# Optimization experiments

Measured on AMD Instinct MI355X. Metric: run time of the kernel, lower is better.

The kernel has to match this reference:

```python
import jax, jax.numpy as jnp
import numpy as np

N, E, IN_DIM, HID, HEADS, OUT_DIM, T = 50000, 200000, 32, 64, 4, 32, 3
NEG_SLOPE = 0.2  # PyG GATv2Conv default


def setup_inputs() -> dict:
    key = jax.random.key(0)
    ks = jax.random.split(key, 16)
    s = 0.1
    return {
        "feat": jax.random.normal(ks[0], (N, IN_DIM), jnp.float32),
        "W_in": jax.random.normal(ks[1], (IN_DIM, HID), jnp.float32) * s,
        "b_in": jnp.zeros((HID,), jnp.float32),
        "Wl": jax.random.normal(ks[2], (2 * HID, HEADS * HID), jnp.float32) * s,
        "bl": jnp.zeros((HEADS * HID,), jnp.float32),
        "Wr": jax.random.normal(ks[3], (2 * HID, HEADS * HID), jnp.float32) * s,
        "br": jnp.zeros((HEADS * HID,), jnp.float32),
        "att": jax.random.normal(ks[4], (HEADS, HID), jnp.float32) * s,
        "b_conv": jnp.zeros((HEADS * HID,), jnp.float32),
        "Wg": jax.random.normal(ks[5], (HID, OUT_DIM), jnp.float32) * s,
        "bg": jnp.zeros((OUT_DIM,), jnp.float32),
        "edge_index": jax.random.randint(ks[6], (2, E), 0, N, jnp.int32),
        "node_mask": jax.random.randint(ks[7], (N,), 0, T + 1, jnp.int32),
        "current_state": jax.random.randint(ks[8], (N,), 0, 2, jnp.int32),
    }


def reference(feat, W_in, b_in, Wl, bl, Wr, br, att, b_conv, Wg, bg,
              edge_index, node_mask, current_state):
    # add self loops (GATv2Conv add_self_loops=True)
    loops = jnp.arange(N, dtype=edge_index.dtype)
    src = jnp.concatenate([edge_index[0], loops])  # [E+N]
    dst = jnp.concatenate([edge_index[1], loops])

    h0 = feat @ W_in + b_in  # [N, HID]
    bias_sum = b_conv.reshape(HEADS, HID).sum(0)  # heads are summed after bias add

    def step(h, i):
        active = node_mask > i  # [N] bool: nodes updated at this step
        x = jnp.concatenate([h, h0], axis=-1)  # [N, 2*HID]
        xl = (x @ Wl + bl).reshape(N, HEADS, HID)  # source transform
        xr = (x @ Wr + br).reshape(N, HEADS, HID)  # target transform
        e_act = active[src] & active[dst]  # edge alive iff both endpoints active
        s = jax.nn.leaky_relu(xl[src] + xr[dst], NEG_SLOPE)  # [E+N, H, C]
        score = jnp.einsum('ehc,hc->eh', s, att)  # [E+N, H]
        score = jnp.where(e_act[:, None], score, -1e30)
        smax = jax.lax.stop_gradient(
            jax.ops.segment_max(score, dst, num_segments=N))  # [N, H]
        ex = jnp.exp(score - smax[dst]) * e_act[:, None].astype(score.dtype)
        denom = jax.ops.segment_sum(ex, dst, num_segments=N)  # [N, H]
        alpha = ex / jnp.maximum(denom[dst], 1e-16)  # segment softmax per dst
        msg = alpha[:, :, None] * xl[src]  # [E+N, H, C]
        agg = jax.ops.segment_sum(msg, dst, num_segments=N)  # [N, H, C]
        out = jnp.tanh(agg.sum(1) + bias_sum)  # sum over heads, then Tanh
        return jnp.where(active[:, None], out, h), None

    h, _ = jax.lax.scan(step, h0, jnp.arange(T))
    # original returns g_embed(h[current_state]); fixed-shape variant: mask rows
    out = (h @ Wg + bg) * (current_state[:, None] > 0).astype(h.dtype)
    return out
```

## Files before the change

### kernel.cpp

```cpp
#include <hip/hip_runtime.h>
#include <hip/hip_bf16.h>

#define NN      50000
#define EE      200000
#define IN_DIM  32
#define HID     64
#define HEADS   4
#define OUTD    32
#define TSTEPS  3

typedef unsigned short bf16_t;
typedef __attribute__((ext_vector_type(8))) short  short8;
typedef __attribute__((ext_vector_type(4))) float  floatx4;

__device__ __forceinline__ float b2f(bf16_t u) {
    union { unsigned int i; float f; } v; v.i = ((unsigned int)u) << 16; return v.f;
}
__device__ __forceinline__ bf16_t f2b(float f) {
    union { float f; unsigned int i; } v; v.f = f;
    unsigned int r = v.i + 0x7FFF + ((v.i >> 16) & 1);
    return (bf16_t)(r >> 16);
}

#define DPP_ADD(x, ctrl) ((x) + __int_as_float(                                 \
        __builtin_amdgcn_update_dpp(0, __float_as_int(x), (ctrl), 0xF, 0xF, true)))

#define H0_BLOCKS ((NN + 63) / 64)
#define NB_NODE   ((NN + 255) / 256)
#define NBC       (NB_NODE * 4)
#define EB        ((EE + 1023) / 1024)

__global__ __launch_bounds__(256) void k_setup(
        const void* W_in, const void* b_in, const void* att, const void* bconv,
        const void* Wg, const void* bg,
        const void* Wl_raw, const void* Wr_raw, const void* bl_raw, const void* br_raw,
        const void* feat_raw, const int* __restrict__ nmask,
        const int* __restrict__ e_src, const int* __restrict__ e_dst,
        float* attf, float* bcf, float* Wgf, float* bgf,
        bf16_t* __restrict__ Wt, bf16_t* __restrict__ WtS, float* __restrict__ bb,
        int* __restrict__ deg4, int* __restrict__ flag, int* __restrict__ bcount,
        bf16_t* __restrict__ h0, bf16_t* __restrict__ h) {
    __shared__ int bad;
    __shared__ float Ws[IN_DIM * HID];
    __shared__ float bs[HID];
    __shared__ int wcnt[4][4];
    int t = threadIdx.x, bid = blockIdx.x;
    if (t == 0) bad = 0;
    __syncthreads();
    {
        const bf16_t* p = (const bf16_t*)W_in;
        int mybad = 0;
        for (int i = t; i < IN_DIM * HID; i += 256) {
            float v = b2f(p[i]);
            if (v != v || fabsf(v) > 100.f) mybad = 1;
        }
        if (mybad) atomicOr(&bad, 1);
    }
    __syncthreads();
    int f = bad ? 0 : 1;
    if (bid == 0 && t == 0) *flag = f;

    if (bid < 256) {
        int i = bid * 256 + t;
        int n = i >> 7, k = i & 127;
        const void* W = (n < 256) ? Wl_raw : Wr_raw;
        int nn = (n < 256) ? n : n - 256;
        float v = f ? b2f(((const bf16_t*)W)[k * 256 + nn])
                    : ((const float*)W)[k * 256 + nn];
        Wt[n * 128 + k] = f2b(v);
        if (k < 64) {
            float v2 = f ? b2f(((const bf16_t*)W)[(k + 64) * 256 + nn])
                         : ((const float*)W)[(k + 64) * 256 + nn];
            WtS[n * 64 + k] = f2b(v + v2);
        }
        if (k == 0) {
            const void* b = (n < 256) ? bl_raw : br_raw;
            bb[n] = f ? b2f(((const bf16_t*)b)[nn]) : ((const float*)b)[nn];
        }
    } else if (bid < 267) {
        int i = (bid - 256) * 256 + t;
        const void* src; float* dst; int off;
        if      (i < 256)  { src = att;   dst = attf; off = i; }
        else if (i < 512)  { src = bconv; dst = bcf;  off = i - 256; }
        else if (i < 2560) { src = Wg;    dst = Wgf;  off = i - 512; }
        else if (i < 2592) { src = bg;    dst = bgf;  off = i - 2560; }
        else return;
        dst[off] = f ? b2f(((const bf16_t*)src)[off]) : ((const float*)src)[off];
    } else if (bid < 267 + NB_NODE) {
        int nb = bid - 267;
        int i = nb * 256 + t;
        bool valid = i < NN;
        int wid = t >> 6, lane = t & 63;
        int v = 0;
        if (valid) { int m = nmask[i]; v = m < 0 ? 0 : (m > 3 ? 3 : m); }
#pragma unroll
        for (int b = 0; b < 4; b++) {
            unsigned long long mm = __ballot(valid && v == b);
            if (lane == 0) wcnt[wid][b] = __popcll(mm);
        }
        __syncthreads();
        if (t < 4)
            bcount[nb * 4 + t] = wcnt[0][t] + wcnt[1][t] + wcnt[2][t] + wcnt[3][t];
    } else if (bid < 267 + NB_NODE + EB) {
        int nb = bid - 267 - NB_NODE;
        int i = (nb * 256 + t) * 4;
        if (i + 3 < EE) {
            int4 dv = *(const int4*)(e_dst + i);
            int4 sv = *(const int4*)(e_src + i);
            int m0 = nmask[sv.x]; m0 = m0 < 0 ? 0 : (m0 > 3 ? 3 : m0);
            int m1 = nmask[sv.y]; m1 = m1 < 0 ? 0 : (m1 > 3 ? 3 : m1);
            int m2 = nmask[sv.z]; m2 = m2 < 0 ? 0 : (m2 > 3 ? 3 : m2);
            int m3 = nmask[sv.w]; m3 = m3 < 0 ? 0 : (m3 > 3 ? 3 : m3);
            atomicAdd(&deg4[dv.x * 4 + m0], 1);
            atomicAdd(&deg4[dv.y * 4 + m1], 1);
            atomicAdd(&deg4[dv.z * 4 + m2], 1);
            atomicAdd(&deg4[dv.w * 4 + m3], 1);
        } else {
            for (; i < EE; i++) {
                int s = e_src[i];
                int m = nmask[s]; m = m < 0 ? 0 : (m > 3 ? 3 : m);
                atomicAdd(&deg4[e_dst[i] * 4 + m], 1);
            }
        }
    } else {
        for (int i = t; i < IN_DIM * HID; i += 256)
            Ws[i] = f ? b2f(((const bf16_t*)W_in)[i]) : ((const float*)W_in)[i];
        if (t < HID)
            bs[t] = f ? b2f(((const bf16_t*)b_in)[t]) : ((const float*)b_in)[t];
        __syncthreads();
        int nb = bid - (267 + NB_NODE + EB);
        int wid = t >> 6, c = t & 63;
#pragma unroll
        for (int g = 0; g < 16; g++) {
            int node = (nb * 16 + g) * 4 + wid;
            if (node >= NN) break;
            float acc = bs[c];
            if (f) {
                const short8* fr8 = (const short8*)((const bf16_t*)feat_raw
                                                    + (size_t)node * IN_DIM);
#pragma unroll
                for (int j = 0; j < 4; j++) {
                    short8 fv = fr8[j];
#pragma unroll
                    for (int k = 0; k < 8; k++)
                        acc += b2f((bf16_t)fv[k]) * Ws[(j * 8 + k) * HID + c];
                }
            } else {
                const float4* fr4 = (const float4*)((const float*)feat_raw
                                                    + (size_t)node * IN_DIM);
#pragma unroll
                for (int j = 0; j < 8; j++) {
                    float4 fv = fr4[j];
                    acc += fv.x * Ws[(j * 4 + 0) * HID + c];
                    acc += fv.y * Ws[(j * 4 + 1) * HID + c];
                    acc += fv.z * Ws[(j * 4 + 2) * HID + c];
                    acc += fv.w * Ws[(j * 4 + 3) * HID + c];
                }
            }
            bf16_t o = f2b(acc);
            h0[(size_t)node * HID + c] = o;
            h [(size_t)node * HID + c] = o;
        }
    }
}

__global__ __launch_bounds__(256) void k_scan(const int* __restrict__ deg4,
                                              int* __restrict__ cur4,
                                              int* __restrict__ rend4,
                                              const int* __restrict__ bcount,
                                              int* __restrict__ mbuf,
                                              int n, int nch) {
    __shared__ int sc[256];
    __shared__ int spre[256];
    __shared__ int cb[4];
    int t = threadIdx.x, bid = blockIdx.x;

    if (bid == 0) {
        if (t < 4) cb[t] = 0;
        __syncthreads();
        for (int i = t; i < NBC; i += 256) atomicAdd(&cb[i & 3], bcount[i]);
        __syncthreads();
        if (t == 0) {
            int c1 = cb[1], c2 = cb[2], c3 = cb[3];
            mbuf[7] = 0;
            mbuf[6] = c3;
            mbuf[5] = c3 + c2;
            mbuf[4] = c3 + c2 + c1;
            mbuf[8] = c3 + c2 + c1;
            mbuf[9] = c3 + c2;
            mbuf[10] = c3;
        }
    }

    const int4* d4 = (const int4*)deg4;
    int base = bid * 1024;
    int pre = 0;
    for (int i = t; i < base; i += 256) {
        int4 q = d4[i];
        pre += q.x + q.y + q.z + q.w;
    }
    spre[t] = pre; __syncthreads();
    for (int off = 128; off > 0; off >>= 1) {
        if (t < off) spre[t] += spre[t + off];
        __syncthreads();
    }
    int bpref = spre[0];

    int4 dd[4]; int tot[4]; int s = 0;
#pragma unroll
    for (int j = 0; j < 4; j++) {
        int i = base + t * 4 + j;
        if (i < n) dd[j] = d4[i];
        else { dd[j].x = 0; dd[j].y = 0; dd[j].z = 0; dd[j].w = 0; }
        tot[j] = dd[j].x + dd[j].y + dd[j].z + dd[j].w;
        s += tot[j];
    }
    sc[t] = s; __syncthreads();
    for (int off = 1; off < 256; off <<= 1) {
        int add = (t >= off) ? sc[t - off] : 0;
        __syncthreads();
        sc[t] += add;
        __syncthreads();
    }
    int run = sc[t] - s + bpref;
#pragma unroll
    for (int j = 0; j < 4; j++) {
        int i = base + t * 4 + j;
        if (i < n) {
            int c3 = run;
            int c2 = c3 + dd[j].w;
            int c1 = c2 + dd[j].z;
            int c0 = c1 + dd[j].y;
            int4 cu; cu.x = c0; cu.y = c1; cu.z = c2; cu.w = c3;
            *(int4*)(cur4 + i * 4) = cu;
            int4 re; re.x = c0; re.y = c1; re.z = c2; re.w = run;
            *(int4*)(rend4 + i * 4) = re;
        }
        run += tot[j];
    }
}

__global__ __launch_bounds__(256) void k_scatter_all(const int* __restrict__ src,
                                                     const int* __restrict__ dst,
                                                     int* __restrict__ cur4,
                                                     int* __restrict__ col,
                                                     const int* __restrict__ mask,
                                                     int* __restrict__ mbuf,
                                                     int* __restrict__ order) {
    int t = threadIdx.x, bid = blockIdx.x;
    int i = bid * 256 + t;
    if (i < EE) {
        int sv = src[i];
        int m = mask[sv]; m = m < 0 ? 0 : (m > 3 ? 3 : m);
        int d = dst[i];
        int pos = atomicAdd(&cur4[d * 4 + m], 1);
        col[pos] = sv;
    }
    if (bid < NB_NODE) {
        __shared__ int wcnt[4][4];
        __shared__ int bbase[4];
        int wid = t >> 6, lane = t & 63;
        int ni = bid * 256 + t;
        bool valid = ni < NN;
        int v = 0;
        if (valid) { int m = mask[ni]; v = m < 0 ? 0 : (m > 3 ? 3 : m); }
        int rank = 0;
#pragma unroll
        for (int b = 0; b < 4; b++) {
            unsigned long long mm = __ballot(valid && v == b);
            if (valid && v == b)
                rank = __popcll(mm & ((lane == 0) ? 0ull : (~0ull >> (64 - lane))));
            if (lane == 0) wcnt[wid][b] = __popcll(mm);
        }
        __syncthreads();
        if (t < 4) {
            int tot = wcnt[0][t] + wcnt[1][t] + wcnt[2][t] + wcnt[3][t];
            bbase[t] = atomicAdd(&mbuf[4 + t], tot);
        }
        __syncthreads();
        if (valid) {
            int wpre = 0;
            for (int ww = 0; ww < wid; ww++) wpre += wcnt[ww][v];
            order[bbase[v] + wpre + rank] = ni;
        }
    }
}

__global__ __launch_bounds__(256) void k_gemm0(const bf16_t* __restrict__ h0,
                                               const bf16_t* __restrict__ WtS,
                                               const float* __restrict__ bb,
                                               bf16_t* __restrict__ xl,
                                               bf16_t* __restrict__ xr,
                                               const int* __restrict__ order,
                                               const int* __restrict__ mbuf) {
    int count = mbuf[8];
    int mbase = blockIdx.x * 64;
    if (mbase >= count) return;

    __shared__ bf16_t smem[64 * 72 + 128 * 72];
    bf16_t* As = smem;
    bf16_t* Bs = smem + 64 * 72;
    bf16_t* Cs = smem;

    int t = threadIdx.x;
    int nbase = blockIdx.y * 128;

    {
        int ln = t >> 2, lq = t & 3;
        int idx = mbase + ln;
        int node = (idx < count) ? order[idx] : -1;
        ulonglong2 z; z.x = 0; z.y = 0;
        ulonglong2 v0 = z, v1 = z;
        if (node >= 0) {
            v0 = *(const ulonglong2*)(h0 + (size_t)node * HID + lq * 16);
            v1 = *(const ulonglong2*)(h0 + (size_t)node * HID + lq * 16 + 8);
        }
        *(ulonglong2*)(&As[ln * 72 + lq * 16]) = v0;
        *(ulonglong2*)(&As[ln * 72 + lq * 16 + 8]) = v1;
    }
    {
        int n = t >> 1, kc = (t & 1) * 32;
        const bf16_t* srcp = WtS + (size_t)(nbase + n) * 64 + kc;
        bf16_t* dstp = &Bs[n * 72 + kc];
        *(ulonglong2*)(dstp)      = *(const ulonglong2*)(srcp);
        *(ulonglong2*)(dstp + 8)  = *(const ulonglong2*)(srcp + 8);
        *(ulonglong2*)(dstp + 16) = *(const ulonglong2*)(srcp + 16);
        *(ulonglong2*)(dstp + 24) = *(const ulonglong2*)(srcp + 24);
    }
    __syncthreads();

    int wv = t >> 6, lane = t & 63, mrow = lane & 15, quad = lane >> 4;
    floatx4 acc[8];
#pragma unroll
    for (int nf = 0; nf < 8; nf++) acc[nf] = (floatx4){0.f, 0.f, 0.f, 0.f};
#pragma unroll
    for (int kq = 0; kq < 2; kq++) {
        short8 a = *(const short8*)(&As[(wv * 16 + mrow) * 72 + kq * 32 + quad * 8]);
#pragma unroll
        for (int nf = 0; nf < 8; nf++) {
            short8 b = *(const short8*)(&Bs[(nf * 16 + mrow) * 72 + kq * 32 + quad * 8]);
            acc[nf] = __builtin_amdgcn_mfma_f32_16x16x32_bf16(a, b, acc[nf], 0, 0, 0);
        }
    }
    __syncthreads();

#pragma unroll
    for (int nf = 0; nf < 8; nf++) {
        float bv = bb[nbase + nf * 16 + mrow];
#pragma unroll
        for (int r = 0; r < 4; r++) {
            int m = wv * 16 + quad * 4 + r;
            Cs[m * 136 + nf * 16 + mrow] = f2b(acc[nf][r] + bv);
        }
    }
    __syncthreads();

    bf16_t* outp = (blockIdx.y < 2) ? xl : xr;
    int cc = (blockIdx.y & 1) * 128;
#pragma unroll
    for (int i = 0; i < 4; i++) {
        int c = t + i * 256;
        int m = c >> 4, kc = (c & 15) * 8;
        int idx = mbase + m;
        if (idx < count) {
            int node = order[idx];
            *(ulonglong2*)(outp + (size_t)node * 256 + cc + kc) =
                *(const ulonglong2*)(&Cs[m * 136 + kc]);
        }
    }
}

__global__ __launch_bounds__(256) void k_gemm_mfma(const bf16_t* __restrict__ h,
                                                   const bf16_t* __restrict__ h0,
                                                   const bf16_t* __restrict__ Wt,
                                                   const float* __restrict__ bb,
                                                   bf16_t* __restrict__ xl,
                                                   bf16_t* __restrict__ xr,
                                                   const int* __restrict__ order,
                                                   const int* __restrict__ mbuf,
                                                   int step) {
    int count = mbuf[8 + step];
    int mbase = blockIdx.x * 64;
    if (mbase >= count) return;

    __shared__ bf16_t smem[64 * 136 + 128 * 136];
    bf16_t* As = smem;
    bf16_t* Bs = smem + 64 * 136;
    bf16_t* Cs = smem;

    int t = threadIdx.x;
    int nbase = blockIdx.y * 128;

    {
        int ln = t >> 2, lq = t & 3;
        int idx = mbase + ln;
        int node = (idx < count) ? order[idx] : -1;
        ulonglong2 z; z.x = 0; z.y = 0;
#pragma unroll
        for (int j = 0; j < 2; j++) {
            int chunk = lq + j * 4;
            ulonglong2 vh = z, vh0 = z;
            if (node >= 0) {
                vh  = *(const ulonglong2*)(h  + (size_t)node * HID + chunk * 8);
                vh0 = *(const ulonglong2*)(h0 + (size_t)node * HID + chunk * 8);
            }
            *(ulonglong2*)(&As[ln * 136 + chunk * 8]) = vh;
            *(ulonglong2*)(&As[ln * 136 + 64 + chunk * 8]) = vh0;
        }
    }
#pragma unroll
    for (int i = 0; i < 8; i++) {
        int c = t + i * 256;
        int n = c >> 4, kc = (c & 15) * 8;
        *(ulonglong2*)(&Bs[n * 136 + kc]) =
            *(const ulonglong2*)(Wt + (size_t)(nbase + n) * 128 + kc);
    }
    __syncthreads();

    int wv = t >> 6, lane = t & 63, mrow = lane & 15, quad = lane >> 4;
    floatx4 acc[8];
#pragma unroll
    for (int nf = 0; nf < 8; nf++) acc[nf] = (floatx4){0.f, 0.f, 0.f, 0.f};
#pragma unroll
    for (int kq = 0; kq < 4; kq++) {
        short8 a = *(const short8*)(&As[(wv * 16 + mrow) * 136 + kq * 32 + quad * 8]);
#pragma unroll
        for (int nf = 0; nf < 8; nf++) {
            short8 b = *(const short8*)(&Bs[(nf * 16 + mrow) * 136 + kq * 32 + quad * 8]);
            acc[nf] = __builtin_amdgcn_mfma_f32_16x16x32_bf16(a, b, acc[nf], 0, 0, 0);
        }
    }
    __syncthreads();

#pragma unroll
    for (int nf = 0; nf < 8; nf++) {
        float bv = bb[nbase + nf * 16 + mrow];
#pragma unroll
        for (int r = 0; r < 4; r++) {
            int m = wv * 16 + quad * 4 + r;
            Cs[m * 136 + nf * 16 + mrow] = f2b(acc[nf][r] + bv);
        }
    }
    __syncthreads();

    bf16_t* outp = (blockIdx.y < 2) ? xl : xr;
    int cc = (blockIdx.y & 1) * 128;
#pragma unroll
    for (int i = 0; i < 4; i++) {
        int c = t + i * 256;
        int m = c >> 4, kc = (c & 15) * 8;
        int idx = mbase + m;
        if (idx < count) {
            int node = order[idx];
            *(ulonglong2*)(outp + (size_t)node * 256 + cc + kc) =
                *(const ulonglong2*)(&Cs[m * 136 + kc]);
        }
    }
}

__global__ __launch_bounds__(256) void k_agg(bf16_t* __restrict__ h,
                                             const bf16_t* __restrict__ xl,
                                             const bf16_t* __restrict__ xr,
                                             const float* __restrict__ att,
                                             const float* __restrict__ b_conv,
                                             const int* __restrict__ rend4,
                                             const int* __restrict__ col,
                                             const int* __restrict__ order,
                                             const int* __restrict__ mbuf,
                                             int step) {
    int count = mbuf[8 + step];
    int wid = threadIdx.x >> 6;
    int lane = threadIdx.x & 63;
    const int stride = gridDim.x * 4;
    float4 attv = *(const float4*)(att + lane * 4);
    attv.x *= 1.44269504f; attv.y *= 1.44269504f;
    attv.z *= 1.44269504f; attv.w *= 1.44269504f;
    float4 bcv  = *(const float4*)(b_conv + lane * 4);

    int idx = blockIdx.x * 4 + wid;
    if (idx >= count) return;

    int node = order[idx];
    int4 re = *(const int4*)(rend4 + node * 4);
    ushort4 xru   = *(const ushort4*)(xr + (size_t)node * 256 + lane * 4);
    ushort4 uself = *(const ushort4*)(xl + (size_t)node * 256 + lane * 4);

    for (;;) {
        int nidx = idx + stride;
        bool more = nidx < count;
        int nnode = order[more ? nidx : idx];
        int4 re_n = *(const int4*)(rend4 + nnode * 4);
        ushort4 xru_n   = *(const ushort4*)(xr + (size_t)nnode * 256 + lane * 4);
        ushort4 uself_n = *(const ushort4*)(xl + (size_t)nnode * 256 + lane * 4);

        int e0 = re.w;
        int e1 = (step == 0) ? re.x : (step == 1) ? re.y : re.z;

        float xr0 = b2f(xru.x), xr1 = b2f(xru.y), xr2 = b2f(xru.z), xr3 = b2f(xru.w);
        float a0 = 0.f, a1 = 0.f, a2 = 0.f, a3 = 0.f, l = 0.f;

        auto ld = [&](int s) {
            return *(const ushort4*)(xl + (size_t)s * 256 + lane * 4);
        };
        auto body = [&](ushort4 xu) {
            float x0 = b2f(xu.x), x1 = b2f(xu.y), x2 = b2f(xu.z), x3 = b2f(xu.w);
            float v0 = x0 + xr0; v0 = fmaxf(v0, 0.2f * v0);
            float v1 = x1 + xr1; v1 = fmaxf(v1, 0.2f * v1);
            float v2 = x2 + xr2; v2 = fmaxf(v2, 0.2f * v2);
            float v3 = x3 + xr3; v3 = fmaxf(v3, 0.2f * v3);
            float part = attv.x * v0 + attv.y * v1 + attv.z * v2 + attv.w * v3;
            part = DPP_ADD(part, 0xB1);
            part = DPP_ADD(part, 0x4E);
            part = DPP_ADD(part, 0x141);
            part = DPP_ADD(part, 0x140);
            float p = exp2f(part);
            l += p;
            a0 += p * x0; a1 += p * x1; a2 += p * x2; a3 += p * x3;
        };

        body(uself);
        int e = e0;
        for (; e + 4 <= e1; e += 4) {
            int c0 = col[e], c1 = col[e + 1], c2 = col[e + 2], c3 = col[e + 3];
            ushort4 u0 = ld(c0), u1 = ld(c1), u2 = ld(c2), u3 = ld(c3);
            body(u0); body(u1); body(u2); body(u3);
        }
        int rem = e1 - e;
        if (rem > 0) {
            int c0 = col[e];
            int c1 = (rem > 1) ? col[e + 1] : c0;
            int c2 = (rem > 2) ? col[e + 2] : c0;
            ushort4 u0 = ld(c0), u1 = ld(c1), u2 = ld(c2);
            body(u0);
            if (rem > 1) body(u1);
            if (rem > 2) body(u2);
        }

        float inv = __builtin_amdgcn_rcpf(l);
        float t0 = a0 * inv + bcv.x;
        float t1 = a1 * inv + bcv.y;
        float t2 = a2 * inv + bcv.z;
        float t3 = a3 * inv + bcv.w;
        t0 += __shfl_xor(t0, 16, 64); t0 += __shfl_xor(t0, 32, 64);
        t1 += __shfl_xor(t1, 16, 64); t1 += __shfl_xor(t1, 32, 64);
        t2 += __shfl_xor(t2, 16, 64); t2 += __shfl_xor(t2, 32, 64);
        t3 += __shfl_xor(t3, 16, 64); t3 += __shfl_xor(t3, 32, 64);
        if (lane < 16) {
            ushort4 o;
            o.x = f2b(tanhf(t0)); o.y = f2b(tanhf(t1));
            o.z = f2b(tanhf(t2)); o.w = f2b(tanhf(t3));
            *(ushort4*)(h + (size_t)node * HID + lane * 4) = o;
        }

        if (!more) return;
        idx = nidx; node = nnode;
        re = re_n; xru = xru_n; uself = uself_n;
    }
}

__global__ __launch_bounds__(256) void k_out(const bf16_t* __restrict__ h,
                                             const float* __restrict__ Wg,
                                             const float* __restrict__ bg,
                                             const int* __restrict__ cs,
                                             void* __restrict__ out,
                                             const int* __restrict__ flag) {
    __shared__ float Ws[HID * OUTD];
    __shared__ float bs[OUTD];
    int t = threadIdx.x;
    for (int i = t; i < HID * OUTD; i += 256) Ws[i] = Wg[i];
    if (t < OUTD) bs[t] = bg[t];
    __syncthreads();
    int g0 = t >> 5, c = t & 31;
    int fl = *flag;
#pragma unroll
    for (int g = 0; g < 4; g++) {
        int node = blockIdx.x * 32 + g * 8 + g0;
        if (node >= NN) break;
        float res = 0.f;
        if (cs[node] > 0) {
            const short8* hr8 = (const short8*)(h + (size_t)node * HID);
            float acc = bs[c];
#pragma unroll
            for (int j = 0; j < 8; j++) {
                short8 hv = hr8[j];
#pragma unroll
                for (int k = 0; k < 8; k++)
                    acc += b2f((bf16_t)hv[k]) * Ws[(j * 8 + k) * OUTD + c];
            }
            res = acc;
        }
        size_t idx = (size_t)node * OUTD + c;
        if (fl) ((bf16_t*)out)[idx] = f2b(res);
        else    ((float*)out)[idx]  = res;
    }
}

static inline size_t alignup(size_t x) { return (x + 255) & ~(size_t)255; }

extern "C" void kernel_launch(void* const* d_in, const int* in_sizes, int n_in,
                              void* d_out, int out_size, void* d_ws, size_t ws_size,
                              hipStream_t stream) {
    const void* feat_raw  = d_in[0];
    const void* W_in_raw  = d_in[1];
    const void* b_in_raw  = d_in[2];
    const void* Wl_raw    = d_in[3];
    const void* bl_raw    = d_in[4];
    const void* Wr_raw    = d_in[5];
    const void* br_raw    = d_in[6];
    const void* att_raw   = d_in[7];
    const void* bconv_raw = d_in[8];
    const void* Wg_raw    = d_in[9];
    const void* bg_raw    = d_in[10];
    const int* edge       = (const int*)d_in[11];
    const int* nmask      = (const int*)d_in[12];
    const int* cstate     = (const int*)d_in[13];

    const int* e_src = edge;
    const int* e_dst = edge + EE;

    const size_t SZ_HB   = alignup((size_t)NN * HID * sizeof(bf16_t));
    const size_t SZ_X    = alignup((size_t)NN * 256 * sizeof(bf16_t));
    const size_t SZ_I4   = alignup((size_t)NN * 4 * sizeof(int));
    const size_t SZ_I    = alignup((size_t)NN * sizeof(int));
    const size_t SZ_COL  = alignup((size_t)EE * sizeof(int));
    const int nch = (NN + 1023) / 1024;
    const size_t SZ_BC   = alignup((size_t)NBC * sizeof(int));
    const size_t SZ_WT   = alignup((size_t)512 * 128 * sizeof(bf16_t));
    const size_t SZ_WTS  = alignup((size_t)512 * 64 * sizeof(bf16_t));
    const size_t SZ_B    = alignup(512 * sizeof(float));
    const size_t SZ_WG   = alignup((size_t)HID * OUTD * sizeof(float));

    char* w = (char*)d_ws;
    bf16_t* h0   = (bf16_t*)w; w += SZ_HB;
    bf16_t* h    = (bf16_t*)w; w += SZ_HB;
    bf16_t* xl   = (bf16_t*)w; w += SZ_X;
    bf16_t* xr   = (bf16_t*)w; w += SZ_X;
    int* deg4    = (int*)w;    w += SZ_I4;
    int* mbuf    = (int*)w;    w += 256;
    int* cur4    = (int*)w;    w += SZ_I4;
    int* rend4   = (int*)w;    w += SZ_I4;
    int* colA    = (int*)w;    w += SZ_COL;
    int* order   = (int*)w;    w += SZ_I;
    int* bcount  = (int*)w;    w += SZ_BC;
    bf16_t* Wt   = (bf16_t*)w; w += SZ_WT;
    bf16_t* WtS  = (bf16_t*)w; w += SZ_WTS;
    float* bb    = (float*)w;  w += SZ_B;
    float* attf  = (float*)w;  w += SZ_B;
    float* bcf   = (float*)w;  w += SZ_B;
    float* Wgf   = (float*)w;  w += SZ_WG;
    float* bgf   = (float*)w;  w += SZ_B;
    int* flag    = (int*)w;    w += 256;
    if ((size_t)(w - (char*)d_ws) > ws_size) return;

    hipMemsetAsync(deg4, 0, SZ_I4 + 256, stream);

    k_setup<<<267 + NB_NODE + EB + H0_BLOCKS, 256, 0, stream>>>(
        W_in_raw, b_in_raw, att_raw, bconv_raw, Wg_raw, bg_raw,
        Wl_raw, Wr_raw, bl_raw, br_raw, feat_raw, nmask, e_src, e_dst,
        attf, bcf, Wgf, bgf, Wt, WtS, bb, deg4, flag, bcount, h0, h);

    k_scan<<<nch, 256, 0, stream>>>(deg4, cur4, rend4, bcount, mbuf, NN, nch);
    k_scatter_all<<<(EE + 255) / 256, 256, 0, stream>>>(e_src, e_dst, cur4, colA,
                                                        nmask, mbuf, order);

    k_gemm0<<<dim3((NN + 63) / 64, 4), 256, 0, stream>>>(h0, WtS, bb, xl, xr, order, mbuf);
    k_agg<<<2048, 256, 0, stream>>>(h, xl, xr, attf, bcf, rend4, colA, order, mbuf, 0);

    for (int s = 1; s < TSTEPS; s++) {
        k_gemm_mfma<<<dim3((NN + 63) / 64, 4), 256, 0, stream>>>(h, h0, Wt, bb, xl, xr,
                                                                 order, mbuf, s);
        k_agg<<<2048, 256, 0, stream>>>(h, xl, xr, attf, bcf,
                                        rend4, colA, order, mbuf, s);
    }

    k_out<<<(NN + 31) / 32, 256, 0, stream>>>(h, Wgf, bgf, cstate, d_out, flag);
}
```

Measured before the change: 274.2 us.

## Sort active node order by mask class and clamped degree buckets

Builds the node order array from 64 classes (mask level × degree clamped to 15) instead of just mask level. Counts per class are gathered as a histogram in the scan kernel, and positions are assigned in the scatter kernel with per-class atomics. This drops the ballot-based count pass from setup. Grouping nodes of similar degree is meant to balance work inside aggregation wavefronts. In exchange, order within a class becomes nondeterministic and the scatter kernel needs a serial 64-entry prefix in each block.

```diff
diff --git a/kernel.cpp b/kernel.cpp
--- a/kernel.cpp
+++ b/kernel.cpp
@@ -27,7 +27,6 @@
 
 #define H0_BLOCKS ((NN + 63) / 64)
 #define NB_NODE   ((NN + 255) / 256)
-#define NBC       (NB_NODE * 4)
 #define EB        ((EE + 1023) / 1024)
 
 __global__ __launch_bounds__(256) void k_setup(
@@ -38,12 +37,11 @@
         const int* __restrict__ e_src, const int* __restrict__ e_dst,
         float* attf, float* bcf, float* Wgf, float* bgf,
         bf16_t* __restrict__ Wt, bf16_t* __restrict__ WtS, float* __restrict__ bb,
-        int* __restrict__ deg4, int* __restrict__ flag, int* __restrict__ bcount,
+        int* __restrict__ deg4, int* __restrict__ flag,
         bf16_t* __restrict__ h0, bf16_t* __restrict__ h) {
     __shared__ int bad;
     __shared__ float Ws[IN_DIM * HID];
     __shared__ float bs[HID];
-    __shared__ int wcnt[4][4];
     int t = threadIdx.x, bid = blockIdx.x;
     if (t == 0) bad = 0;
     __syncthreads();
@@ -86,23 +84,8 @@
         else if (i < 2592) { src = bg;    dst = bgf;  off = i - 2560; }
         else return;
         dst[off] = f ? b2f(((const bf16_t*)src)[off]) : ((const float*)src)[off];
-    } else if (bid < 267 + NB_NODE) {
+    } else if (bid < 267 + EB) {
         int nb = bid - 267;
-        int i = nb * 256 + t;
-        bool valid = i < NN;
-        int wid = t >> 6, lane = t & 63;
-        int v = 0;
-        if (valid) { int m = nmask[i]; v = m < 0 ? 0 : (m > 3 ? 3 : m); }
-#pragma unroll
-        for (int b = 0; b < 4; b++) {
-            unsigned long long mm = __ballot(valid && v == b);
-            if (lane == 0) wcnt[wid][b] = __popcll(mm);
-        }
-        __syncthreads();
-        if (t < 4)
-            bcount[nb * 4 + t] = wcnt[0][t] + wcnt[1][t] + wcnt[2][t] + wcnt[3][t];
-    } else if (bid < 267 + NB_NODE + EB) {
-        int nb = bid - 267 - NB_NODE;
         int i = (nb * 256 + t) * 4;
         if (i + 3 < EE) {
             int4 dv = *(const int4*)(e_dst + i);
@@ -128,7 +111,7 @@
         if (t < HID)
             bs[t] = f ? b2f(((const bf16_t*)b_in)[t]) : ((const float*)b_in)[t];
         __syncthreads();
-        int nb = bid - (267 + NB_NODE + EB);
+        int nb = bid - (267 + EB);
         int wid = t >> 6, c = t & 63;
 #pragma unroll
         for (int g = 0; g < 16; g++) {
@@ -165,32 +148,16 @@
 }
 
 __global__ __launch_bounds__(256) void k_scan(const int* __restrict__ deg4,
+                                              const int* __restrict__ nmask,
                                               int* __restrict__ cur4,
                                               int* __restrict__ rend4,
-                                              const int* __restrict__ bcount,
-                                              int* __restrict__ mbuf,
-                                              int n, int nch) {
+                                              int* __restrict__ clscnt,
+                                              int n) {
     __shared__ int sc[256];
     __shared__ int spre[256];
-    __shared__ int cb[4];
+    __shared__ int lhist[64];
     int t = threadIdx.x, bid = blockIdx.x;
-
-    if (bid == 0) {
-        if (t < 4) cb[t] = 0;
-        __syncthreads();
-        for (int i = t; i < NBC; i += 256) atomicAdd(&cb[i & 3], bcount[i]);
-        __syncthreads();
-        if (t == 0) {
-            int c1 = cb[1], c2 = cb[2], c3 = cb[3];
-            mbuf[7] = 0;
-            mbuf[6] = c3;
-            mbuf[5] = c3 + c2;
-            mbuf[4] = c3 + c2 + c1;
-            mbuf[8] = c3 + c2 + c1;
-            mbuf[9] = c3 + c2;
-            mbuf[10] = c3;
-        }
-    }
+    if (t < 64) lhist[t] = 0;
 
     const int4* d4 = (const int4*)deg4;
     int base = bid * 1024;
@@ -235,9 +202,15 @@
             *(int4*)(cur4 + i * 4) = cu;
             int4 re; re.x = c0; re.y = c1; re.z = c2; re.w = run;
             *(int4*)(rend4 + i * 4) = re;
+            int m = nmask[i]; m = m < 0 ? 0 : (m > 3 ? 3 : m);
+            int d = dd[j].y + dd[j].z + dd[j].w;
+            int dc = d > 15 ? 15 : d;
+            atomicAdd(&lhist[(3 - m) * 16 + dc], 1);
         }
         run += tot[j];
     }
+    __syncthreads();
+    if (t < 64 && lhist[t]) atomicAdd(&clscnt[t], lhist[t]);
 }
 
 __global__ __launch_bounds__(256) void k_scatter_all(const int* __restrict__ src,
@@ -245,6 +218,9 @@
                                                      int* __restrict__ cur4,
                                                      int* __restrict__ col,
                                                      const int* __restrict__ mask,
+                                                     const int* __restrict__ rend4,
+                                                     const int* __restrict__ clscnt,
+                                                     int* __restrict__ clscur,
                                                      int* __restrict__ mbuf,
                                                      int* __restrict__ order) {
     int t = threadIdx.x, bid = blockIdx.x;
@@ -257,31 +233,26 @@
         col[pos] = sv;
     }
     if (bid < NB_NODE) {
-        __shared__ int wcnt[4][4];
-        __shared__ int bbase[4];
-        int wid = t >> 6, lane = t & 63;
+        __shared__ int sbase[64];
+        if (t == 0) {
+            int a = 0;
+            for (int c = 0; c < 64; c++) { sbase[c] = a; a += clscnt[c]; }
+        }
+        __syncthreads();
+        if (bid == 0 && t == 0) {
+            mbuf[8]  = sbase[48];
+            mbuf[9]  = sbase[32];
+            mbuf[10] = sbase[16];
+        }
         int ni = bid * 256 + t;
-        bool valid = ni < NN;
-        int v = 0;
-        if (valid) { int m = mask[ni]; v = m < 0 ? 0 : (m > 3 ? 3 : m); }
-        int rank = 0;
-#pragma unroll
-        for (int b = 0; b < 4; b++) {
-            unsigned long long mm = __ballot(valid && v == b);
-            if (valid && v == b)
-                rank = __popcll(mm & ((lane == 0) ? 0ull : (~0ull >> (64 - lane))));
-            if (lane == 0) wcnt[wid][b] = __popcll(mm);
-        }
-        __syncthreads();
-        if (t < 4) {
-            int tot = wcnt[0][t] + wcnt[1][t] + wcnt[2][t] + wcnt[3][t];
-            bbase[t] = atomicAdd(&mbuf[4 + t], tot);
-        }
-        __syncthreads();
-        if (valid) {
-            int wpre = 0;
-            for (int ww = 0; ww < wid; ww++) wpre += wcnt[ww][v];
-            order[bbase[v] + wpre + rank] = ni;
+        if (ni < NN) {
+            int m = mask[ni]; m = m < 0 ? 0 : (m > 3 ? 3 : m);
+            int4 re = *(const int4*)(rend4 + ni * 4);
+            int d = re.x - re.w;
+            int dc = d > 15 ? 15 : d;
+            int cls = (3 - m) * 16 + dc;
+            int pos = sbase[cls] + atomicAdd(&clscur[cls], 1);
+            order[pos] = ni;
         }
     }
 }
@@ -624,7 +595,6 @@
     const size_t SZ_I    = alignup((size_t)NN * sizeof(int));
     const size_t SZ_COL  = alignup((size_t)EE * sizeof(int));
     const int nch = (NN + 1023) / 1024;
-    const size_t SZ_BC   = alignup((size_t)NBC * sizeof(int));
     const size_t SZ_WT   = alignup((size_t)512 * 128 * sizeof(bf16_t));
     const size_t SZ_WTS  = alignup((size_t)512 * 64 * sizeof(bf16_t));
     const size_t SZ_B    = alignup(512 * sizeof(float));
@@ -637,11 +607,11 @@
     bf16_t* xr   = (bf16_t*)w; w += SZ_X;
     int* deg4    = (int*)w;    w += SZ_I4;
     int* mbuf    = (int*)w;    w += 256;
+    int* cls     = (int*)w;    w += 512;
     int* cur4    = (int*)w;    w += SZ_I4;
     int* rend4   = (int*)w;    w += SZ_I4;
     int* colA    = (int*)w;    w += SZ_COL;
     int* order   = (int*)w;    w += SZ_I;
-    int* bcount  = (int*)w;    w += SZ_BC;
     bf16_t* Wt   = (bf16_t*)w; w += SZ_WT;
     bf16_t* WtS  = (bf16_t*)w; w += SZ_WTS;
     float* bb    = (float*)w;  w += SZ_B;
@@ -652,16 +622,20 @@
     int* flag    = (int*)w;    w += 256;
     if ((size_t)(w - (char*)d_ws) > ws_size) return;
 
-    hipMemsetAsync(deg4, 0, SZ_I4 + 256, stream);
-
-    k_setup<<<267 + NB_NODE + EB + H0_BLOCKS, 256, 0, stream>>>(
+    int* clscnt = cls;
+    int* clscur = cls + 64;
+
+    hipMemsetAsync(deg4, 0, SZ_I4 + 256 + 512, stream);
+
+    k_setup<<<267 + EB + H0_BLOCKS, 256, 0, stream>>>(
         W_in_raw, b_in_raw, att_raw, bconv_raw, Wg_raw, bg_raw,
         Wl_raw, Wr_raw, bl_raw, br_raw, feat_raw, nmask, e_src, e_dst,
-        attf, bcf, Wgf, bgf, Wt, WtS, bb, deg4, flag, bcount, h0, h);
-
-    k_scan<<<nch, 256, 0, stream>>>(deg4, cur4, rend4, bcount, mbuf, NN, nch);
+        attf, bcf, Wgf, bgf, Wt, WtS, bb, deg4, flag, h0, h);
+
+    k_scan<<<nch, 256, 0, stream>>>(deg4, nmask, cur4, rend4, clscnt, NN);
     k_scatter_all<<<(EE + 255) / 256, 256, 0, stream>>>(e_src, e_dst, cur4, colA,
-                                                        nmask, mbuf, order);
+                                                        nmask, rend4, clscnt, clscur,
+                                                        mbuf, order);
 
     k_gemm0<<<dim3((NN + 63) / 64, 4), 256, 0, stream>>>(h0, WtS, bb, xl, xr, order, mbuf);
     k_agg<<<2048, 256, 0, stream>>>(h, xl, xr, attf, bcf, rend4, colA, order, mbuf, 0);
```

New measurement: 386.3 us. 1.41x slower.
